# Kernel optimization log

Hardware: AMD Instinct MI355X
Metric: run time of the kernel (lower is better)

## Reference

```python
import jax, jax.numpy as jnp
import numpy as np

N_NODES = 100000
N_EDGES = 1600000
DIN = 128
DOUT = 128
N_SUP = 2


def setup_inputs() -> dict:
    key = jax.random.key(0)
    k = jax.random.split(key, 6)
    x = jax.random.normal(k[0], (N_NODES, DIN), dtype=jnp.float32)
    w = jax.random.normal(k[1], (N_SUP, DIN, DOUT), dtype=jnp.float32) * (1.0 / np.sqrt(DIN))
    bias = jax.random.normal(k[2], (DOUT,), dtype=jnp.float32) * 0.01
    sup_vals = jax.random.uniform(k[3], (N_SUP, N_EDGES), dtype=jnp.float32)
    sup_rows = jax.random.randint(k[4], (N_SUP, N_EDGES), 0, N_NODES, dtype=jnp.int32)
    sup_cols = jax.random.randint(k[5], (N_SUP, N_EDGES), 0, N_NODES, dtype=jnp.int32)
    return {"x": x, "w": w, "bias": bias, "sup_vals": sup_vals,
            "sup_rows": sup_rows, "sup_cols": sup_cols}


def _spmm(vals, rows, cols, dense):
    # COO sparse [N,N] @ dense [N,D] -> [N,D]
    gathered = vals[:, None] * dense[cols]        # [E, D]
    return jax.ops.segment_sum(gathered, rows, num_segments=N_NODES)


def reference(x, w, bias, sup_vals, sup_rows, sup_cols):
    # pre_sup_i = x @ w_i for each support: [S, N, Dout]
    pre = jnp.einsum('nd,sdo->sno', x, w)
    # SpMM per support, vmapped over the support axis, then summed
    supports = jax.vmap(_spmm)(sup_vals, sup_rows, sup_cols, pre)  # [S, N, Dout]
    out = supports.sum(axis=0) + bias
    return jax.nn.relu(out)
```

## Files before the change

### kernel.cpp

```cpp
#include <hip/hip_runtime.h>

#define N_NODES 100000
#define N_EDGES 1600000
#define DIN 128
#define DOUT 128
#define N_SUP 2
#define E_TOT (N_SUP * N_EDGES)

#define BIN_ROWS 128
#define BSHIFT 7
#define NBINS ((N_NODES + BIN_ROWS - 1) / BIN_ROWS)
#define CAP 4608

#define SC_EPT 16
#define SC_BLOCK 256
#define SC_CHUNK (SC_EPT * SC_BLOCK)
#define NBLK_SC ((E_TOT + SC_CHUNK - 1) / SC_CHUNK)

#define GEMM_ROWS 128
#define NBLK_GEMM ((N_NODES + GEMM_ROWS - 1) / GEMM_ROWS)
#define LDK 136
#define GEMM_SMEM (2 * GEMM_ROWS * LDK * 2)
#define SORT_SMEM (CAP * 8 + 2 * BIN_ROWS * 4)
#define SCAT_SMEM (2 * NBINS * 4)

typedef float        f32x2 __attribute__((ext_vector_type(2)));
typedef float        f32x4 __attribute__((ext_vector_type(4)));
typedef unsigned int u32;
typedef u32          u32x2 __attribute__((ext_vector_type(2)));
typedef u32          u32x4 __attribute__((ext_vector_type(4)));
typedef short        bf16x8 __attribute__((ext_vector_type(8)));

static __device__ __forceinline__ u32 pack_bf16x2(float lo, float hi) {
    u32 ul = __float_as_uint(lo);
    u32 uh = __float_as_uint(hi);
    ul = (ul + 0x7FFFu + ((ul >> 16) & 1u)) >> 16;
    uh = ((uh + 0x7FFFu + ((uh >> 16) & 1u)) >> 16) << 16;
    return ul | uh;
}

static __device__ __forceinline__ void gemm_body(char* smem, int bidx, int s,
                                                 const float* __restrict__ x,
                                                 const u32* __restrict__ wTb,
                                                 u32* __restrict__ pre) {
    typedef unsigned short (*stage_p)[GEMM_ROWS][LDK];
    stage_p stage = (stage_p)smem;
    float (*epi)[129] = (float (*)[129])smem;

    const int row0 = bidx * GEMM_ROWS;
    const int t = threadIdx.x;
    const int lane = t & 63;
    const int wv = t >> 6;

    {
        const int r = t >> 1;
        const int half = t & 1;
        const int gr = row0 + r;
        u32* dst = (u32*)&stage[0][r][half * 64];
        u32 o[32];
        if (gr < N_NODES) {
            const float* p = x + (size_t)gr * DIN + half * 64;
            #pragma unroll
            for (int j = 0; j < 16; j++) {
                const f32x4 a = *(const f32x4*)(p + j * 4);
                o[2 * j]     = pack_bf16x2(a.x, a.y);
                o[2 * j + 1] = pack_bf16x2(a.z, a.w);
            }
        } else {
            #pragma unroll
            for (int j = 0; j < 32; j++) o[j] = 0;
        }
        #pragma unroll
        for (int j = 0; j < 8; j++)
            *(u32x4*)(dst + j * 4) = *(u32x4*)&o[j * 4];
        const u32* wp = wTb + ((size_t)s * 128 + r) * 64 + half * 32;
        u32* wdst = (u32*)&stage[1][r][half * 64];
        #pragma unroll
        for (int j = 0; j < 8; j++)
            *(u32x4*)(wdst + j * 4) = *(const u32x4*)(wp + j * 4);
    }
    __syncthreads();

    const int q = lane >> 4;
    const int ml = lane & 15;
    const int m0 = wv * 32;

    f32x4 acc[2][8];
    #pragma unroll
    for (int mt = 0; mt < 2; mt++)
        #pragma unroll
        for (int nt = 0; nt < 8; nt++) acc[mt][nt] = (f32x4){0.f, 0.f, 0.f, 0.f};

    #pragma unroll
    for (int kt = 0; kt < 4; kt++) {
        const int k0 = kt * 32 + q * 8;
        const bf16x8 a0 = *(const bf16x8*)&stage[0][m0 + ml][k0];
        const bf16x8 a1 = *(const bf16x8*)&stage[0][m0 + 16 + ml][k0];
        #pragma unroll
        for (int nt = 0; nt < 8; nt++) {
            const bf16x8 b = *(const bf16x8*)&stage[1][nt * 16 + ml][k0];
            acc[0][nt] = __builtin_amdgcn_mfma_f32_16x16x32_bf16(a0, b, acc[0][nt], 0, 0, 0);
            acc[1][nt] = __builtin_amdgcn_mfma_f32_16x16x32_bf16(a1, b, acc[1][nt], 0, 0, 0);
        }
    }
    __syncthreads();

    #pragma unroll
    for (int mt = 0; mt < 2; mt++)
        #pragma unroll
        for (int nt = 0; nt < 8; nt++)
            #pragma unroll
            for (int r = 0; r < 4; r++)
                epi[m0 + mt * 16 + q * 4 + r][nt * 16 + ml] = acc[mt][nt][r];
    __syncthreads();

    {
        const int row = t >> 1;
        const int half = t & 1;
        const int gr = row0 + row;
        if (gr < N_NODES) {
            u32 ov[32];
            #pragma unroll
            for (int j = 0; j < 32; j++)
                ov[j] = pack_bf16x2(epi[row][half * 64 + 2 * j],
                                    epi[row][half * 64 + 2 * j + 1]);
            u32* op = pre + ((size_t)s * N_NODES + gr) * 64 + half * 32;
            #pragma unroll
            for (int j = 0; j < 8; j++)
                __builtin_nontemporal_store(*(u32x4*)&ov[j * 4], (u32x4*)(op + j * 4));
        }
    }
}

static __device__ __forceinline__ void scatter_body(char* smem, int bidx,
                                                    const int* __restrict__ rows,
                                                    const int* __restrict__ cols,
                                                    const float* __restrict__ vals,
                                                    int* __restrict__ bin_cursor,
                                                    u32x2* __restrict__ edata) {
    int* lcnt = (int*)smem;
    int* lbase = lcnt + NBINS;
    const int t = threadIdx.x;
    for (int i = t; i < NBINS; i += 256) lcnt[i] = 0;
    __syncthreads();

    const int base = bidx * SC_CHUNK;
    int bin[SC_EPT], lpos[SC_EPT];
    u32x2 pay[SC_EPT];
    #pragma unroll
    for (int j = 0; j < SC_EPT; j++) {
        const int i = base + j * 256 + t;
        if (i < E_TOT) {
            const int r = __builtin_nontemporal_load(rows + i);
            const int c = __builtin_nontemporal_load(cols + i);
            const float v = __builtin_nontemporal_load(vals + i);
            const int b = r >> BSHIFT;
            bin[j] = b;
            lpos[j] = atomicAdd(&lcnt[b], 1);
            pay[j].x = (u32)(c + ((i >= N_EDGES) ? N_NODES : 0)) |
                       ((u32)(r & (BIN_ROWS - 1)) << 18);
            pay[j].y = __float_as_uint(v);
        } else {
            bin[j] = -1;
        }
    }
    __syncthreads();
    for (int b = t; b < NBINS; b += 256) {
        const int c = lcnt[b];
        if (c) lbase[b] = b * CAP + atomicAdd(&bin_cursor[b], c);
    }
    __syncthreads();
    #pragma unroll
    for (int j = 0; j < SC_EPT; j++) {
        if (bin[j] >= 0) edata[lbase[bin[j]] + lpos[j]] = pay[j];
    }
}

static __device__ __forceinline__ void sort_body(char* smem, int b,
                                                 u32x2* __restrict__ edata,
                                                 const int* __restrict__ bin_cursor,
                                                 int2* __restrict__ rbe) {
    u32x2* ebuf = (u32x2*)smem;
    int* rcnt = (int*)(smem + CAP * 8);
    int* rscan = rcnt + BIN_ROWS;
    const int t = threadIdx.x;
    const int beg = b * CAP;
    const int cnt = min(bin_cursor[b], CAP);

    for (int e = t; e < cnt; e += 256)
        ebuf[e] = __builtin_nontemporal_load(edata + beg + e);
    if (t < BIN_ROWS) rcnt[t] = 0;
    __syncthreads();

    for (int e = t; e < cnt; e += 256)
        atomicAdd(&rcnt[ebuf[e].x >> 18], 1);
    __syncthreads();

    const int v = (t < BIN_ROWS) ? rcnt[t] : 0;
    if (t < BIN_ROWS) rscan[t] = v;
    __syncthreads();
    #pragma unroll
    for (int off = 1; off < BIN_ROWS; off <<= 1) {
        const int u = (t < BIN_ROWS && t >= off) ? rscan[t - off] : 0;
        __syncthreads();
        if (t < BIN_ROWS) rscan[t] += u;
        __syncthreads();
    }
    if (t < BIN_ROWS) {
        const int ex = rscan[t] - v;
        rcnt[t] = ex;
        const int row = b * BIN_ROWS + t;
        if (row < N_NODES) {
            int2 be;
            be.x = beg + ex;
            be.y = beg + ex + v;
            rbe[row] = be;
        }
    }
    __syncthreads();
    for (int e = t; e < cnt; e += 256) {
        const u32x2 d = ebuf[e];
        const int pos = beg + atomicAdd(&rcnt[d.x >> 18], 1);
        u32x2 o;
        o.x = d.x & 0x3FFFFu;
        o.y = d.y;
        edata[pos] = o;
    }
}

__global__ __launch_bounds__(256) void scatwconv_kernel(const float* __restrict__ w,
                                                        u32* __restrict__ wTb,
                                                        const int* __restrict__ rows,
                                                        const int* __restrict__ cols,
                                                        const float* __restrict__ vals,
                                                        int* __restrict__ bin_cursor,
                                                        u32x2* __restrict__ edata) {
    __shared__ alignas(16) char smem[SCAT_SMEM];
    const int bid = blockIdx.x;
    if (bid < N_SUP) {
        const int s = bid;
        const int n = threadIdx.x >> 1;
        const int kh = (threadIdx.x & 1) * 64;
        const float* wp = w + (size_t)s * DIN * DOUT + n;
        u32 o[32];
        #pragma unroll
        for (int j = 0; j < 32; j++) {
            const float lo = wp[(size_t)(kh + 2 * j) * DOUT];
            const float hi = wp[(size_t)(kh + 2 * j + 1) * DOUT];
            o[j] = pack_bf16x2(lo, hi);
        }
        u32* op = wTb + ((size_t)s * 128 + n) * 64 + kh / 2;
        #pragma unroll
        for (int j = 0; j < 8; j++)
            *(u32x4*)(op + j * 4) = *(u32x4*)&o[j * 4];
        return;
    }
    scatter_body(smem, bid - N_SUP, rows, cols, vals, bin_cursor, edata);
}

__global__ __launch_bounds__(256) void gemmsort_kernel(const float* __restrict__ x,
                                                       const u32* __restrict__ wTb,
                                                       u32* __restrict__ pre,
                                                       u32x2* __restrict__ edata,
                                                       const int* __restrict__ bin_cursor,
                                                       int2* __restrict__ rbe) {
    __shared__ alignas(16) char smem[GEMM_SMEM];
    const int bid = blockIdx.x;
    const int kind = bid % 3;
    const int idx = bid / 3;
    if (kind == 2) sort_body(smem, idx, edata, bin_cursor, rbe);
    else           gemm_body(smem, idx, kind, x, wTb, pre);
}

__global__ __launch_bounds__(256, 6) void gather_kernel(const u32* __restrict__ pre,
                                                        const u32x2* __restrict__ edata,
                                                        const int2* __restrict__ rbe,
                                                        const float* __restrict__ bias,
                                                        float* __restrict__ out) {
    const int lane = threadIdx.x & 63;
    const int wid = threadIdx.x >> 6;
    const int row = blockIdx.x * 4 + wid;
    if (row >= N_NODES) return;

    const int2 be = rbe[row];
    int e = be.x;
    const int end = be.y;

    float ax = 0.f, ay = 0.f;

    if (e + 8 <= end) {
        u32x2 d[8];
        #pragma unroll
        for (int j = 0; j < 8; j++)
            d[j] = __builtin_nontemporal_load(edata + e + j);
        for (;;) {
            u32 u[8];
            #pragma unroll
            for (int j = 0; j < 8; j++)
                u[j] = pre[(u32)((d[j].x << 6) + (u32)lane)];
            const int en = e + 8;
            const bool more = (en + 8 <= end);
            u32x2 dn[8];
            if (more) {
                #pragma unroll
                for (int j = 0; j < 8; j++)
                    dn[j] = __builtin_nontemporal_load(edata + en + j);
            }
            #pragma unroll
            for (int j = 0; j < 8; j++) {
                const float v = __uint_as_float(d[j].y);
                ax = fmaf(v, __uint_as_float(u[j] << 16), ax);
                ay = fmaf(v, __uint_as_float(u[j] & 0xFFFF0000u), ay);
            }
            e = en;
            if (!more) break;
            #pragma unroll
            for (int j = 0; j < 8; j++) d[j] = dn[j];
        }
    }
    for (; e + 4 <= end; e += 4) {
        u32x2 d[4];
        #pragma unroll
        for (int j = 0; j < 4; j++)
            d[j] = __builtin_nontemporal_load(edata + e + j);
        u32 u[4];
        #pragma unroll
        for (int j = 0; j < 4; j++)
            u[j] = pre[(u32)((d[j].x << 6) + (u32)lane)];
        #pragma unroll
        for (int j = 0; j < 4; j++) {
            const float v = __uint_as_float(d[j].y);
            ax = fmaf(v, __uint_as_float(u[j] << 16), ax);
            ay = fmaf(v, __uint_as_float(u[j] & 0xFFFF0000u), ay);
        }
    }
    for (; e < end; e++) {
        const u32x2 d = __builtin_nontemporal_load(edata + e);
        const u32 u = pre[(u32)((d.x << 6) + (u32)lane)];
        const float v = __uint_as_float(d.y);
        ax = fmaf(v, __uint_as_float(u << 16), ax);
        ay = fmaf(v, __uint_as_float(u & 0xFFFF0000u), ay);
    }

    const float2 b = *(const float2*)(bias + lane * 2);
    f32x2 r;
    r.x = fmaxf(ax + b.x, 0.f);
    r.y = fmaxf(ay + b.y, 0.f);
    __builtin_nontemporal_store(r, (f32x2*)(out + (size_t)row * DOUT + lane * 2));
}

extern "C" void kernel_launch(void* const* d_in, const int* in_sizes, int n_in,
                              void* d_out, int out_size, void* d_ws, size_t ws_size,
                              hipStream_t stream) {
    (void)in_sizes; (void)n_in; (void)out_size; (void)ws_size;
    const float* x        = (const float*)d_in[0];
    const float* w        = (const float*)d_in[1];
    const float* bias     = (const float*)d_in[2];
    const float* sup_vals = (const float*)d_in[3];
    const int*   sup_rows = (const int*)d_in[4];
    const int*   sup_cols = (const int*)d_in[5];
    float* out = (float*)d_out;

    char* ws = (char*)d_ws;
    u32*   pre       = (u32*)ws;
    u32x2* edata     = (u32x2*)(ws + (size_t)N_SUP * N_NODES * 64 * 4);
    int2*  rbe       = (int2*)((char*)edata + (size_t)NBINS * CAP * 8);
    int*   bin_cursor= (int*)(rbe + N_NODES);
    u32*   wTb       = (u32*)(bin_cursor + NBINS + 2);

    (void)hipMemsetAsync(bin_cursor, 0, NBINS * sizeof(int), stream);
    scatwconv_kernel<<<N_SUP + NBLK_SC, 256, 0, stream>>>(w, wTb, sup_rows, sup_cols,
                                                          sup_vals, bin_cursor, edata);
    gemmsort_kernel<<<3 * NBLK_GEMM, 256, 0, stream>>>(x, wTb, pre, edata,
                                                       bin_cursor, rbe);
    gather_kernel<<<(N_NODES + 3) / 4, 256, 0, stream>>>(pre, edata, rbe, bias, out);
}
```

Measured before the change: 363.8 us.

## Compute both supports per GEMM block and drop second atomic pass in bin sort

Each GEMM block now converts its x tile to bf16 once and multiplies it by both support weights in turn, reusing the staged A tile instead of launching a separate block per support. This halves the x reads and bf16 conversions, and the grid goes from 3 to 2 blocks per GEMM tile. The bin sort now keeps each edge's local slot from the counting atomic and adds the scanned row base, so the second round of LDS atomics is gone. In exchange each GEMM thread holds twice as many accumulator registers, which may lower occupancy, and the epilogue needs extra barriers.

```diff
diff --git a/kernel.cpp b/kernel.cpp
--- a/kernel.cpp
+++ b/kernel.cpp
@@ -11,6 +11,7 @@
 #define BSHIFT 7
 #define NBINS ((N_NODES + BIN_ROWS - 1) / BIN_ROWS)
 #define CAP 4608
+#define EPT_BS (CAP / 256)
 
 #define SC_EPT 16
 #define SC_BLOCK 256
@@ -21,7 +22,6 @@
 #define NBLK_GEMM ((N_NODES + GEMM_ROWS - 1) / GEMM_ROWS)
 #define LDK 136
 #define GEMM_SMEM (2 * GEMM_ROWS * LDK * 2)
-#define SORT_SMEM (CAP * 8 + 2 * BIN_ROWS * 4)
 #define SCAT_SMEM (2 * NBINS * 4)
 
 typedef float        f32x2 __attribute__((ext_vector_type(2)));
@@ -39,7 +39,7 @@
     return ul | uh;
 }
 
-static __device__ __forceinline__ void gemm_body(char* smem, int bidx, int s,
+static __device__ __forceinline__ void gemm_body(char* smem, int bidx,
                                                  const float* __restrict__ x,
                                                  const u32* __restrict__ wTb,
                                                  u32* __restrict__ pre) {
@@ -51,11 +51,11 @@
     const int t = threadIdx.x;
     const int lane = t & 63;
     const int wv = t >> 6;
+    const int r = t >> 1;
+    const int half = t & 1;
+    const int gr = row0 + r;
 
     {
-        const int r = t >> 1;
-        const int half = t & 1;
-        const int gr = row0 + r;
         u32* dst = (u32*)&stage[0][r][half * 64];
         u32 o[32];
         if (gr < N_NODES) {
@@ -73,7 +73,7 @@
         #pragma unroll
         for (int j = 0; j < 8; j++)
             *(u32x4*)(dst + j * 4) = *(u32x4*)&o[j * 4];
-        const u32* wp = wTb + ((size_t)s * 128 + r) * 64 + half * 32;
+        const u32* wp = wTb + (size_t)r * 64 + half * 32;
         u32* wdst = (u32*)&stage[1][r][half * 64];
         #pragma unroll
         for (int j = 0; j < 8; j++)
@@ -85,11 +85,14 @@
     const int ml = lane & 15;
     const int m0 = wv * 32;
 
-    f32x4 acc[2][8];
+    f32x4 acc0[2][8], acc1[2][8];
     #pragma unroll
     for (int mt = 0; mt < 2; mt++)
         #pragma unroll
-        for (int nt = 0; nt < 8; nt++) acc[mt][nt] = (f32x4){0.f, 0.f, 0.f, 0.f};
+        for (int nt = 0; nt < 8; nt++) {
+            acc0[mt][nt] = (f32x4){0.f, 0.f, 0.f, 0.f};
+            acc1[mt][nt] = (f32x4){0.f, 0.f, 0.f, 0.f};
+        }
 
     #pragma unroll
     for (int kt = 0; kt < 4; kt++) {
@@ -99,36 +102,58 @@
         #pragma unroll
         for (int nt = 0; nt < 8; nt++) {
             const bf16x8 b = *(const bf16x8*)&stage[1][nt * 16 + ml][k0];
-            acc[0][nt] = __builtin_amdgcn_mfma_f32_16x16x32_bf16(a0, b, acc[0][nt], 0, 0, 0);
-            acc[1][nt] = __builtin_amdgcn_mfma_f32_16x16x32_bf16(a1, b, acc[1][nt], 0, 0, 0);
-        }
-    }
-    __syncthreads();
-
-    #pragma unroll
-    for (int mt = 0; mt < 2; mt++)
-        #pragma unroll
-        for (int nt = 0; nt < 8; nt++)
-            #pragma unroll
-            for (int r = 0; r < 4; r++)
-                epi[m0 + mt * 16 + q * 4 + r][nt * 16 + ml] = acc[mt][nt][r];
+            acc0[0][nt] = __builtin_amdgcn_mfma_f32_16x16x32_bf16(a0, b, acc0[0][nt], 0, 0, 0);
+            acc0[1][nt] = __builtin_amdgcn_mfma_f32_16x16x32_bf16(a1, b, acc0[1][nt], 0, 0, 0);
+        }
+    }
     __syncthreads();
 
     {
-        const int row = t >> 1;
-        const int half = t & 1;
-        const int gr = row0 + row;
+        const u32* wp = wTb + ((size_t)128 + r) * 64 + half * 32;
+        u32* wdst = (u32*)&stage[1][r][half * 64];
+        #pragma unroll
+        for (int j = 0; j < 8; j++)
+            *(u32x4*)(wdst + j * 4) = *(const u32x4*)(wp + j * 4);
+    }
+    __syncthreads();
+
+    #pragma unroll
+    for (int kt = 0; kt < 4; kt++) {
+        const int k0 = kt * 32 + q * 8;
+        const bf16x8 a0 = *(const bf16x8*)&stage[0][m0 + ml][k0];
+        const bf16x8 a1 = *(const bf16x8*)&stage[0][m0 + 16 + ml][k0];
+        #pragma unroll
+        for (int nt = 0; nt < 8; nt++) {
+            const bf16x8 b = *(const bf16x8*)&stage[1][nt * 16 + ml][k0];
+            acc1[0][nt] = __builtin_amdgcn_mfma_f32_16x16x32_bf16(a0, b, acc1[0][nt], 0, 0, 0);
+            acc1[1][nt] = __builtin_amdgcn_mfma_f32_16x16x32_bf16(a1, b, acc1[1][nt], 0, 0, 0);
+        }
+    }
+    __syncthreads();
+
+    #pragma unroll
+    for (int s = 0; s < 2; s++) {
+        #pragma unroll
+        for (int mt = 0; mt < 2; mt++)
+            #pragma unroll
+            for (int nt = 0; nt < 8; nt++)
+                #pragma unroll
+                for (int rr = 0; rr < 4; rr++)
+                    epi[m0 + mt * 16 + q * 4 + rr][nt * 16 + ml] =
+                        (s == 0) ? acc0[mt][nt][rr] : acc1[mt][nt][rr];
+        __syncthreads();
         if (gr < N_NODES) {
             u32 ov[32];
             #pragma unroll
             for (int j = 0; j < 32; j++)
-                ov[j] = pack_bf16x2(epi[row][half * 64 + 2 * j],
-                                    epi[row][half * 64 + 2 * j + 1]);
+                ov[j] = pack_bf16x2(epi[r][half * 64 + 2 * j],
+                                    epi[r][half * 64 + 2 * j + 1]);
             u32* op = pre + ((size_t)s * N_NODES + gr) * 64 + half * 32;
             #pragma unroll
             for (int j = 0; j < 8; j++)
                 __builtin_nontemporal_store(*(u32x4*)&ov[j * 4], (u32x4*)(op + j * 4));
         }
+        __syncthreads();
     }
 }
 
@@ -182,7 +207,7 @@
                                                  int2* __restrict__ rbe) {
     u32x2* ebuf = (u32x2*)smem;
     int* rcnt = (int*)(smem + CAP * 8);
-    int* rscan = rcnt + BIN_ROWS;
+    int* rbase = rcnt + BIN_ROWS;
     const int t = threadIdx.x;
     const int beg = b * CAP;
     const int cnt = min(bin_cursor[b], CAP);
@@ -192,23 +217,27 @@
     if (t < BIN_ROWS) rcnt[t] = 0;
     __syncthreads();
 
-    for (int e = t; e < cnt; e += 256)
-        atomicAdd(&rcnt[ebuf[e].x >> 18], 1);
+    int lp[EPT_BS];
+    #pragma unroll
+    for (int k = 0; k < EPT_BS; k++) {
+        const int e = t + k * 256;
+        if (e < cnt) lp[k] = atomicAdd(&rcnt[ebuf[e].x >> 18], 1);
+    }
     __syncthreads();
 
     const int v = (t < BIN_ROWS) ? rcnt[t] : 0;
-    if (t < BIN_ROWS) rscan[t] = v;
+    if (t < BIN_ROWS) rbase[t] = v;
     __syncthreads();
     #pragma unroll
     for (int off = 1; off < BIN_ROWS; off <<= 1) {
-        const int u = (t < BIN_ROWS && t >= off) ? rscan[t - off] : 0;
+        const int u = (t < BIN_ROWS && t >= off) ? rbase[t - off] : 0;
         __syncthreads();
-        if (t < BIN_ROWS) rscan[t] += u;
+        if (t < BIN_ROWS) rbase[t] += u;
         __syncthreads();
     }
     if (t < BIN_ROWS) {
-        const int ex = rscan[t] - v;
-        rcnt[t] = ex;
+        const int ex = rbase[t] - v;
+        rbase[t] = ex;
         const int row = b * BIN_ROWS + t;
         if (row < N_NODES) {
             int2 be;
@@ -218,13 +247,17 @@
         }
     }
     __syncthreads();
-    for (int e = t; e < cnt; e += 256) {
-        const u32x2 d = ebuf[e];
-        const int pos = beg + atomicAdd(&rcnt[d.x >> 18], 1);
-        u32x2 o;
-        o.x = d.x & 0x3FFFFu;
-        o.y = d.y;
-        edata[pos] = o;
+    #pragma unroll
+    for (int k = 0; k < EPT_BS; k++) {
+        const int e = t + k * 256;
+        if (e < cnt) {
+            const u32x2 d = ebuf[e];
+            const int pos = beg + rbase[d.x >> 18] + lp[k];
+            u32x2 o;
+            o.x = d.x & 0x3FFFFu;
+            o.y = d.y;
+            edata[pos] = o;
+        }
     }
 }
 
@@ -266,10 +299,8 @@
                                                        int2* __restrict__ rbe) {
     __shared__ alignas(16) char smem[GEMM_SMEM];
     const int bid = blockIdx.x;
-    const int kind = bid % 3;
-    const int idx = bid / 3;
-    if (kind == 2) sort_body(smem, idx, edata, bin_cursor, rbe);
-    else           gemm_body(smem, idx, kind, x, wTb, pre);
+    if (bid & 1) sort_body(smem, bid >> 1, edata, bin_cursor, rbe);
+    else         gemm_body(smem, bid >> 1, x, wTb, pre);
 }
 
 __global__ __launch_bounds__(256, 6) void gather_kernel(const u32* __restrict__ pre,
@@ -371,7 +402,7 @@
     (void)hipMemsetAsync(bin_cursor, 0, NBINS * sizeof(int), stream);
     scatwconv_kernel<<<N_SUP + NBLK_SC, 256, 0, stream>>>(w, wTb, sup_rows, sup_cols,
                                                           sup_vals, bin_cursor, edata);
-    gemmsort_kernel<<<3 * NBLK_GEMM, 256, 0, stream>>>(x, wTb, pre, edata,
+    gemmsort_kernel<<<2 * NBLK_GEMM, 256, 0, stream>>>(x, wTb, pre, edata,
                                                        bin_cursor, rbe);
     gather_kernel<<<(N_NODES + 3) / 4, 256, 0, stream>>>(pre, edata, rbe, bias, out);
 }
```

Measured after the change: 393.7 us. +8.2%, slower.
